# Optimization experiments

Hardware: AMD Instinct MI355X
Metric: run time of the kernel (lower is better)

## Reference

```python
import jax, jax.numpy as jnp
import numpy as np

N = 200000
D = 64
NNZ = 6400000
NUM_LAYERS = 4
CURVE = 1.0
MIN_NORM = 1e-15
EPS = 1e-7  # float32 clamp eps for arcosh domain


def logmap0_hyperboloid(x, c):
    # Lorentz-model log map at the origin (HGCN Hyperboloid.logmap0).
    # x: [N, D] points on hyperboloid; first coord is the time component.
    K = 1.0 / c
    sqrtK = K ** 0.5
    y = x[:, 1:]                                             # [N, D-1]
    y_norm = jnp.maximum(
        jnp.linalg.norm(y, axis=-1, keepdims=True), MIN_NORM)
    theta = jnp.maximum(x[:, 0:1] / sqrtK, 1.0 + EPS)
    res = sqrtK * jnp.arccosh(theta) * y / y_norm            # [N, D-1]
    return jnp.concatenate([jnp.zeros_like(x[:, :1]), res], axis=-1)


def spmm(rows, cols, vals, x):
    # COO sparse [N,N] @ dense [N,D]
    return jax.ops.segment_sum(vals[:, None] * x[cols], rows, num_segments=N)


def setup_inputs() -> dict:
    key = jax.random.key(0)
    k1, k2, k3, k4 = jax.random.split(key, 4)
    # Build valid hyperboloid points: x0 = sqrt(K + ||y||^2)
    y = jax.random.normal(k1, (N, D - 1), dtype=jnp.float32)
    K = 1.0 / CURVE
    x0 = jnp.sqrt(K + jnp.sum(y * y, axis=-1, keepdims=True))
    x = jnp.concatenate([x0, y], axis=-1)                    # [N, D]
    rows = jax.random.randint(k2, (NNZ,), 0, N, dtype=jnp.int32)
    cols = jax.random.randint(k3, (NNZ,), 0, N, dtype=jnp.int32)
    vals = jax.random.uniform(k4, (NNZ,), dtype=jnp.float32) / 32.0
    return {"x": x, "rows": rows, "cols": cols, "vals": vals}


def reference(x, rows, cols, vals):
    h = logmap0_hyperboloid(x, CURVE)
    # denseGCN: output[0]=h; output[i+1] = sum(output[1:i+1]) + A @ output[i]
    # Maintain running sum S = sum(output[1:i+1]) instead of re-summing (O(L) not O(L^2)).
    prev = h          # output[i]
    S = jnp.zeros_like(h)
    for i in range(NUM_LAYERS):
        cur = S + spmm(rows, cols, vals, prev) if i > 0 else spmm(rows, cols, vals, prev)
        S = S + cur
        prev = cur
    return prev
```

## Files before the change

### kernel.cpp

```cpp
#include <hip/hip_runtime.h>
#include <hip/hip_fp16.h>

#define SCAN_T 256
#define DELTA 512
#define LOG_DELTA 9
#define CAP 20480
#define PA_CHUNK 8192
#define MAXB 512

__global__ void compute_h_kernel(const float* __restrict__ x, __half2* __restrict__ h, int N) {
    int hw = (blockIdx.x * blockDim.x + threadIdx.x) >> 5;
    if (hw >= N) return;
    int l = threadIdx.x & 31;
    const float2* x2 = (const float2*)x;
    float2 v = x2[hw * 32 + l];
    float y2 = (l == 0) ? v.y * v.y : v.x * v.x + v.y * v.y;
    #pragma unroll
    for (int m = 16; m >= 1; m >>= 1) y2 += __shfl_xor(y2, m, 32);
    float x0 = __shfl(v.x, 0, 32);
    float ynorm = fmaxf(sqrtf(y2), 1e-15f);
    float theta = fmaxf(x0, 1.0f + 1e-7f);
    float alpha = acoshf(theta) / ynorm;
    float2 r = (l == 0) ? make_float2(0.0f, v.y * alpha)
                        : make_float2(v.x * alpha, v.y * alpha);
    h[hw * 32 + l] = __float22half2_rn(r);
}

__device__ __forceinline__ int block_incl_scan(int x) {
    __shared__ int sh[SCAN_T];
    int t = threadIdx.x;
    sh[t] = x; __syncthreads();
    for (int ofs = 1; ofs < SCAN_T; ofs <<= 1) {
        int y = (t >= ofs) ? sh[t - ofs] : 0;
        __syncthreads();
        x += y; sh[t] = x;
        __syncthreads();
    }
    return x;
}

__global__ void pass_a_kernel(const int* __restrict__ rows, const int* __restrict__ cols,
                              const float* __restrict__ vals, int* __restrict__ fill,
                              unsigned long long* __restrict__ slab, int nnz, int NB) {
    __shared__ int cnt[MAXB];
    __shared__ int cur[MAXB];
    int t = threadIdx.x;
    int start = blockIdx.x * PA_CHUNK;
    int end = min(start + PA_CHUNK, nnz);
    for (int i = t; i < NB; i += 256) cnt[i] = 0;
    __syncthreads();
    for (int e = start + t; e < end; e += 256)
        atomicAdd(&cnt[rows[e] >> LOG_DELTA], 1);
    __syncthreads();
    for (int i = t; i < NB; i += 256) {
        int c = cnt[i];
        cur[i] = (c > 0) ? atomicAdd(&fill[i], c) : 0;
    }
    __syncthreads();
    for (int e = start + t; e < end; e += 256) {
        int r = rows[e];
        int bkt = r >> LOG_DELTA;
        int lr = r & (DELTA - 1);
        int pos = atomicAdd(&cur[bkt], 1);
        if (pos < CAP) {
            unsigned long long hi = ((unsigned long long)(((unsigned)lr << 18) | (unsigned)cols[e])) << 32;
            slab[(size_t)bkt * CAP + pos] = hi | (unsigned long long)__float_as_uint(vals[e]);
        }
    }
}

__global__ void bucket_scan_kernel(const int* __restrict__ fill, int* __restrict__ csr_base,
                                   int* __restrict__ row_ptr, int NB, int N, int nnz) {
    int t = threadIdx.x;
    int a0 = (2 * t < NB) ? fill[2 * t] : 0;
    int a1 = (2 * t + 1 < NB) ? fill[2 * t + 1] : 0;
    int s = a0 + a1;
    int incl = block_incl_scan(s);
    int excl = incl - s;
    if (2 * t < NB) csr_base[2 * t] = excl;
    if (2 * t + 1 < NB) csr_base[2 * t + 1] = excl + a0;
    if (t == 0) row_ptr[N] = nnz;
}

__global__ void pass_b_kernel(const int* __restrict__ fill, const unsigned long long* __restrict__ slab,
                              const int* __restrict__ csr_base, unsigned long long* __restrict__ edges,
                              int* __restrict__ row_ptr, int N) {
    __shared__ int cnt[DELTA];
    int b = blockIdx.x;
    int t = threadIdx.x;
    cnt[t] = 0; cnt[t + 256] = 0;
    __syncthreads();
    int m = fill[b];
    if (m > CAP) m = CAP;
    const unsigned long long* sl = slab + (size_t)b * CAP;
    for (int e = t; e < m; e += 256)
        atomicAdd(&cnt[(int)(sl[e] >> 50)], 1);
    __syncthreads();
    int a0 = cnt[2 * t], a1 = cnt[2 * t + 1];
    int s = a0 + a1;
    int incl = block_incl_scan(s);
    int excl = incl - s;
    cnt[2 * t] = excl; cnt[2 * t + 1] = excl + a0;
    __syncthreads();
    int base_row = b * DELTA;
    int cb = csr_base[b];
    for (int lr = t; lr < DELTA; lr += 256) {
        int row = base_row + lr;
        if (row < N) row_ptr[row] = cb + cnt[lr];
    }
    __syncthreads();
    for (int e = t; e < m; e += 256) {
        unsigned long long u = sl[e];
        int lr = (int)(u >> 50);
        unsigned col = (unsigned)(u >> 32) & 0x3FFFFu;
        unsigned vb = (unsigned)u;
        int pos = cb + atomicAdd(&cnt[lr], 1);
        edges[pos] = ((unsigned long long)vb << 32) | col;
    }
}

__global__ void spmm_layer_kernel(const int* __restrict__ row_ptr,
                                  const unsigned long long* __restrict__ edges,
                                  const __half2* __restrict__ pin, __half2* __restrict__ pout,
                                  float2* __restrict__ out, float coef, int init_out,
                                  int store_p, int N) {
    int hw = (blockIdx.x * blockDim.x + threadIdx.x) >> 5;
    if (hw >= N) return;
    int l = threadIdx.x & 31;
    int j = row_ptr[hw];
    int end = row_ptr[hw + 1];
    float accx = 0.0f, accy = 0.0f;
    for (; j + 8 <= end; j += 8) {
        unsigned long long e0 = __builtin_nontemporal_load(&edges[j]);
        unsigned long long e1 = __builtin_nontemporal_load(&edges[j + 1]);
        unsigned long long e2 = __builtin_nontemporal_load(&edges[j + 2]);
        unsigned long long e3 = __builtin_nontemporal_load(&edges[j + 3]);
        unsigned long long e4 = __builtin_nontemporal_load(&edges[j + 4]);
        unsigned long long e5 = __builtin_nontemporal_load(&edges[j + 5]);
        unsigned long long e6 = __builtin_nontemporal_load(&edges[j + 6]);
        unsigned long long e7 = __builtin_nontemporal_load(&edges[j + 7]);
        float2 f0 = __half22float2(pin[(int)(e0 & 0xFFFFFFFFu) * 32 + l]);
        float2 f1 = __half22float2(pin[(int)(e1 & 0xFFFFFFFFu) * 32 + l]);
        float2 f2 = __half22float2(pin[(int)(e2 & 0xFFFFFFFFu) * 32 + l]);
        float2 f3 = __half22float2(pin[(int)(e3 & 0xFFFFFFFFu) * 32 + l]);
        float2 f4 = __half22float2(pin[(int)(e4 & 0xFFFFFFFFu) * 32 + l]);
        float2 f5 = __half22float2(pin[(int)(e5 & 0xFFFFFFFFu) * 32 + l]);
        float2 f6 = __half22float2(pin[(int)(e6 & 0xFFFFFFFFu) * 32 + l]);
        float2 f7 = __half22float2(pin[(int)(e7 & 0xFFFFFFFFu) * 32 + l]);
        float v0 = __int_as_float((int)(e0 >> 32)), v1 = __int_as_float((int)(e1 >> 32));
        float v2 = __int_as_float((int)(e2 >> 32)), v3 = __int_as_float((int)(e3 >> 32));
        float v4 = __int_as_float((int)(e4 >> 32)), v5 = __int_as_float((int)(e5 >> 32));
        float v6 = __int_as_float((int)(e6 >> 32)), v7 = __int_as_float((int)(e7 >> 32));
        accx = fmaf(v0, f0.x, accx); accy = fmaf(v0, f0.y, accy);
        accx = fmaf(v1, f1.x, accx); accy = fmaf(v1, f1.y, accy);
        accx = fmaf(v2, f2.x, accx); accy = fmaf(v2, f2.y, accy);
        accx = fmaf(v3, f3.x, accx); accy = fmaf(v3, f3.y, accy);
        accx = fmaf(v4, f4.x, accx); accy = fmaf(v4, f4.y, accy);
        accx = fmaf(v5, f5.x, accx); accy = fmaf(v5, f5.y, accy);
        accx = fmaf(v6, f6.x, accx); accy = fmaf(v6, f6.y, accy);
        accx = fmaf(v7, f7.x, accx); accy = fmaf(v7, f7.y, accy);
    }
    for (; j < end; ++j) {
        unsigned long long e = __builtin_nontemporal_load(&edges[j]);
        float2 f = __half22float2(pin[(int)(e & 0xFFFFFFFFu) * 32 + l]);
        float v = __int_as_float((int)(e >> 32));
        accx = fmaf(v, f.x, accx); accy = fmaf(v, f.y, accy);
    }
    int idx = hw * 32 + l;
    if (store_p) pout[idx] = __float22half2_rn(make_float2(accx, accy));
    if (init_out) {
        out[idx] = make_float2(coef * accx, coef * accy);
    } else {
        float2 o = out[idx];
        o.x = fmaf(coef, accx, o.x);
        o.y = fmaf(coef, accy, o.y);
        out[idx] = o;
    }
}

extern "C" void kernel_launch(void* const* d_in, const int* in_sizes, int n_in,
                              void* d_out, int out_size, void* d_ws, size_t ws_size,
                              hipStream_t stream) {
    const float* x    = (const float*)d_in[0];
    const int*   rows = (const int*)d_in[1];
    const int*   cols = (const int*)d_in[2];
    const float* vals = (const float*)d_in[3];
    float2* out = (float2*)d_out;
    const int D = 64;
    const int N = in_sizes[0] / D;
    const int nnz = in_sizes[1];
    const int NB = (N + DELTA - 1) / DELTA;

    char* ws = (char*)d_ws;
    size_t off = 0;
    auto alloc = [&](size_t bytes) -> void* {
        void* p = ws + off;
        off = (off + bytes + 255) & ~(size_t)255;
        return p;
    };
    int*     fill     = (int*)alloc((size_t)MAXB * 4);
    int*     csr_base = (int*)alloc((size_t)MAXB * 4);
    int*     row_ptr  = (int*)alloc((size_t)(N + 1) * 4);
    unsigned long long* slab  = (unsigned long long*)alloc((size_t)NB * CAP * 8);
    unsigned long long* edges = (unsigned long long*)alloc((size_t)nnz * 8);
    __half2* pA = (__half2*)alloc((size_t)N * D * 2);
    __half2* pB = (__half2*)alloc((size_t)N * D * 2);
    (void)ws_size; (void)n_in; (void)out_size;

    hipMemsetAsync(fill, 0, (size_t)MAXB * 4, stream);

    const int rblocks = (N + 7) / 8;
    compute_h_kernel<<<rblocks, 256, 0, stream>>>(x, pA, N);

    int pa_blocks = (nnz + PA_CHUNK - 1) / PA_CHUNK;
    pass_a_kernel<<<pa_blocks, 256, 0, stream>>>(rows, cols, vals, fill, slab, nnz, NB);
    bucket_scan_kernel<<<1, 256, 0, stream>>>(fill, csr_base, row_ptr, NB, N, nnz);
    pass_b_kernel<<<NB, 256, 0, stream>>>(fill, slab, csr_base, edges, row_ptr, N);

    spmm_layer_kernel<<<rblocks, 256, 0, stream>>>(row_ptr, edges, pA, pB, out, 4.0f, 1, 1, N);
    spmm_layer_kernel<<<rblocks, 256, 0, stream>>>(row_ptr, edges, pB, pA, out, 5.0f, 0, 1, N);
    spmm_layer_kernel<<<rblocks, 256, 0, stream>>>(row_ptr, edges, pA, pB, out, 3.0f, 0, 1, N);
    spmm_layer_kernel<<<rblocks, 256, 0, stream>>>(row_ptr, edges, pB, pA, out, 1.0f, 0, 0, N);
}
```

Measured before the change: 1.027 ms.

## Sort edges by column phase within rows and fuse output accumulation into final layer

Pass B now bins each row's edges by a coarse column range (32 phases), so edges within a row are ordered by column region. Neighbouring rows processed at the same time then gather from similar parts of the feature table, which should improve cache locality. The per-layer fp32 output read-modify-write is removed: the intermediate half-precision layer results are kept in three buffers, and the final kernel combines them with coefficients 4, 5 and 3. The cost is a 16K-entry shared-memory histogram with a serial 64-element scan per thread, plus one extra workspace buffer.

```diff
diff --git a/kernel.cpp b/kernel.cpp
--- a/kernel.cpp
+++ b/kernel.cpp
@@ -7,6 +7,10 @@
 #define CAP 20480
 #define PA_CHUNK 8192
 #define MAXB 512
+#define NPH 32
+#define PHSHIFT 13
+
+typedef unsigned long long u64;
 
 __global__ void compute_h_kernel(const float* __restrict__ x, __half2* __restrict__ h, int N) {
     int hw = (blockIdx.x * blockDim.x + threadIdx.x) >> 5;
@@ -41,7 +45,7 @@
 
 __global__ void pass_a_kernel(const int* __restrict__ rows, const int* __restrict__ cols,
                               const float* __restrict__ vals, int* __restrict__ fill,
-                              unsigned long long* __restrict__ slab, int nnz, int NB) {
+                              u64* __restrict__ slab, int nnz, int NB) {
     __shared__ int cnt[MAXB];
     __shared__ int cur[MAXB];
     int t = threadIdx.x;
@@ -63,8 +67,8 @@
         int lr = r & (DELTA - 1);
         int pos = atomicAdd(&cur[bkt], 1);
         if (pos < CAP) {
-            unsigned long long hi = ((unsigned long long)(((unsigned)lr << 18) | (unsigned)cols[e])) << 32;
-            slab[(size_t)bkt * CAP + pos] = hi | (unsigned long long)__float_as_uint(vals[e]);
+            u64 hi = ((u64)(((unsigned)lr << 18) | (unsigned)cols[e])) << 32;
+            slab[(size_t)bkt * CAP + pos] = hi | (u64)__float_as_uint(vals[e]);
         }
     }
 }
@@ -82,63 +86,65 @@
     if (t == 0) row_ptr[N] = nnz;
 }
 
-__global__ void pass_b_kernel(const int* __restrict__ fill, const unsigned long long* __restrict__ slab,
-                              const int* __restrict__ csr_base, unsigned long long* __restrict__ edges,
+__global__ void pass_b_kernel(const int* __restrict__ fill, const u64* __restrict__ slab,
+                              const int* __restrict__ csr_base, u64* __restrict__ edges,
                               int* __restrict__ row_ptr, int N) {
-    __shared__ int cnt[DELTA];
+    __shared__ int bins[DELTA * NPH];
     int b = blockIdx.x;
     int t = threadIdx.x;
-    cnt[t] = 0; cnt[t + 256] = 0;
+    for (int i = t; i < DELTA * NPH; i += 256) bins[i] = 0;
     __syncthreads();
     int m = fill[b];
     if (m > CAP) m = CAP;
-    const unsigned long long* sl = slab + (size_t)b * CAP;
-    for (int e = t; e < m; e += 256)
-        atomicAdd(&cnt[(int)(sl[e] >> 50)], 1);
-    __syncthreads();
-    int a0 = cnt[2 * t], a1 = cnt[2 * t + 1];
-    int s = a0 + a1;
+    const u64* sl = slab + (size_t)b * CAP;
+    for (int e = t; e < m; e += 256) {
+        u64 u = sl[e];
+        int lr = (int)(u >> 50);
+        int col = (int)((u >> 32) & 0x3FFFFu);
+        atomicAdd(&bins[lr * NPH + (col >> PHSHIFT)], 1);
+    }
+    __syncthreads();
+    int base = t * 64;
+    int s = 0;
+    #pragma unroll 4
+    for (int k = 0; k < 64; ++k) s += bins[base + k];
     int incl = block_incl_scan(s);
-    int excl = incl - s;
-    cnt[2 * t] = excl; cnt[2 * t + 1] = excl + a0;
-    __syncthreads();
+    int run = incl - s;
+    for (int k = 0; k < 64; ++k) { int c = bins[base + k]; bins[base + k] = run; run += c; }
+    __syncthreads();
+    int cb = csr_base[b];
     int base_row = b * DELTA;
-    int cb = csr_base[b];
     for (int lr = t; lr < DELTA; lr += 256) {
         int row = base_row + lr;
-        if (row < N) row_ptr[row] = cb + cnt[lr];
+        if (row < N) row_ptr[row] = cb + bins[lr * NPH];
     }
     __syncthreads();
     for (int e = t; e < m; e += 256) {
-        unsigned long long u = sl[e];
+        u64 u = sl[e];
         int lr = (int)(u >> 50);
         unsigned col = (unsigned)(u >> 32) & 0x3FFFFu;
         unsigned vb = (unsigned)u;
-        int pos = cb + atomicAdd(&cnt[lr], 1);
-        edges[pos] = ((unsigned long long)vb << 32) | col;
-    }
-}
-
-__global__ void spmm_layer_kernel(const int* __restrict__ row_ptr,
-                                  const unsigned long long* __restrict__ edges,
-                                  const __half2* __restrict__ pin, __half2* __restrict__ pout,
-                                  float2* __restrict__ out, float coef, int init_out,
-                                  int store_p, int N) {
-    int hw = (blockIdx.x * blockDim.x + threadIdx.x) >> 5;
-    if (hw >= N) return;
-    int l = threadIdx.x & 31;
+        int pos = cb + atomicAdd(&bins[lr * NPH + (int)(col >> PHSHIFT)], 1);
+        edges[pos] = ((u64)vb << 32) | col;
+    }
+}
+
+__device__ __forceinline__ void spmm_row(const int* __restrict__ row_ptr,
+                                         const u64* __restrict__ edges,
+                                         const __half2* __restrict__ pin,
+                                         int hw, int l, float& accx, float& accy) {
     int j = row_ptr[hw];
     int end = row_ptr[hw + 1];
-    float accx = 0.0f, accy = 0.0f;
+    accx = 0.0f; accy = 0.0f;
     for (; j + 8 <= end; j += 8) {
-        unsigned long long e0 = __builtin_nontemporal_load(&edges[j]);
-        unsigned long long e1 = __builtin_nontemporal_load(&edges[j + 1]);
-        unsigned long long e2 = __builtin_nontemporal_load(&edges[j + 2]);
-        unsigned long long e3 = __builtin_nontemporal_load(&edges[j + 3]);
-        unsigned long long e4 = __builtin_nontemporal_load(&edges[j + 4]);
-        unsigned long long e5 = __builtin_nontemporal_load(&edges[j + 5]);
-        unsigned long long e6 = __builtin_nontemporal_load(&edges[j + 6]);
-        unsigned long long e7 = __builtin_nontemporal_load(&edges[j + 7]);
+        u64 e0 = __builtin_nontemporal_load(&edges[j]);
+        u64 e1 = __builtin_nontemporal_load(&edges[j + 1]);
+        u64 e2 = __builtin_nontemporal_load(&edges[j + 2]);
+        u64 e3 = __builtin_nontemporal_load(&edges[j + 3]);
+        u64 e4 = __builtin_nontemporal_load(&edges[j + 4]);
+        u64 e5 = __builtin_nontemporal_load(&edges[j + 5]);
+        u64 e6 = __builtin_nontemporal_load(&edges[j + 6]);
+        u64 e7 = __builtin_nontemporal_load(&edges[j + 7]);
         float2 f0 = __half22float2(pin[(int)(e0 & 0xFFFFFFFFu) * 32 + l]);
         float2 f1 = __half22float2(pin[(int)(e1 & 0xFFFFFFFFu) * 32 + l]);
         float2 f2 = __half22float2(pin[(int)(e2 & 0xFFFFFFFFu) * 32 + l]);
@@ -161,21 +167,38 @@
         accx = fmaf(v7, f7.x, accx); accy = fmaf(v7, f7.y, accy);
     }
     for (; j < end; ++j) {
-        unsigned long long e = __builtin_nontemporal_load(&edges[j]);
+        u64 e = __builtin_nontemporal_load(&edges[j]);
         float2 f = __half22float2(pin[(int)(e & 0xFFFFFFFFu) * 32 + l]);
         float v = __int_as_float((int)(e >> 32));
         accx = fmaf(v, f.x, accx); accy = fmaf(v, f.y, accy);
     }
+}
+
+__global__ void spmm_kernel(const int* __restrict__ row_ptr, const u64* __restrict__ edges,
+                            const __half2* __restrict__ pin, __half2* __restrict__ pout, int N) {
+    int hw = (blockIdx.x * blockDim.x + threadIdx.x) >> 5;
+    if (hw >= N) return;
+    int l = threadIdx.x & 31;
+    float accx, accy;
+    spmm_row(row_ptr, edges, pin, hw, l, accx, accy);
+    pout[hw * 32 + l] = __float22half2_rn(make_float2(accx, accy));
+}
+
+__global__ void spmm_final_kernel(const int* __restrict__ row_ptr, const u64* __restrict__ edges,
+                                  const __half2* __restrict__ p1, const __half2* __restrict__ p2,
+                                  const __half2* __restrict__ p3, float2* __restrict__ out, int N) {
+    int hw = (blockIdx.x * blockDim.x + threadIdx.x) >> 5;
+    if (hw >= N) return;
+    int l = threadIdx.x & 31;
+    float accx, accy;
+    spmm_row(row_ptr, edges, p3, hw, l, accx, accy);
     int idx = hw * 32 + l;
-    if (store_p) pout[idx] = __float22half2_rn(make_float2(accx, accy));
-    if (init_out) {
-        out[idx] = make_float2(coef * accx, coef * accy);
-    } else {
-        float2 o = out[idx];
-        o.x = fmaf(coef, accx, o.x);
-        o.y = fmaf(coef, accy, o.y);
-        out[idx] = o;
-    }
+    float2 f1 = __half22float2(p1[idx]);
+    float2 f2 = __half22float2(p2[idx]);
+    float2 f3 = __half22float2(p3[idx]);
+    float ox = fmaf(4.0f, f1.x, fmaf(5.0f, f2.x, fmaf(3.0f, f3.x, accx)));
+    float oy = fmaf(4.0f, f1.y, fmaf(5.0f, f2.y, fmaf(3.0f, f3.y, accy)));
+    out[idx] = make_float2(ox, oy);
 }
 
 extern "C" void kernel_launch(void* const* d_in, const int* in_sizes, int n_in,
@@ -201,24 +224,25 @@
     int*     fill     = (int*)alloc((size_t)MAXB * 4);
     int*     csr_base = (int*)alloc((size_t)MAXB * 4);
     int*     row_ptr  = (int*)alloc((size_t)(N + 1) * 4);
-    unsigned long long* slab  = (unsigned long long*)alloc((size_t)NB * CAP * 8);
-    unsigned long long* edges = (unsigned long long*)alloc((size_t)nnz * 8);
-    __half2* pA = (__half2*)alloc((size_t)N * D * 2);
-    __half2* pB = (__half2*)alloc((size_t)N * D * 2);
+    u64*     slab     = (u64*)alloc((size_t)NB * CAP * 8);
+    u64*     edges    = (u64*)alloc((size_t)nnz * 8);
+    __half2* B0 = (__half2*)alloc((size_t)N * D * 2);
+    __half2* B1 = (__half2*)alloc((size_t)N * D * 2);
+    __half2* B2 = (__half2*)alloc((size_t)N * D * 2);
     (void)ws_size; (void)n_in; (void)out_size;
 
     hipMemsetAsync(fill, 0, (size_t)MAXB * 4, stream);
 
     const int rblocks = (N + 7) / 8;
-    compute_h_kernel<<<rblocks, 256, 0, stream>>>(x, pA, N);
+    compute_h_kernel<<<rblocks, 256, 0, stream>>>(x, B0, N);
 
     int pa_blocks = (nnz + PA_CHUNK - 1) / PA_CHUNK;
     pass_a_kernel<<<pa_blocks, 256, 0, stream>>>(rows, cols, vals, fill, slab, nnz, NB);
     bucket_scan_kernel<<<1, 256, 0, stream>>>(fill, csr_base, row_ptr, NB, N, nnz);
     pass_b_kernel<<<NB, 256, 0, stream>>>(fill, slab, csr_base, edges, row_ptr, N);
 
-    spmm_layer_kernel<<<rblocks, 256, 0, stream>>>(row_ptr, edges, pA, pB, out, 4.0f, 1, 1, N);
-    spmm_layer_kernel<<<rblocks, 256, 0, stream>>>(row_ptr, edges, pB, pA, out, 5.0f, 0, 1, N);
-    spmm_layer_kernel<<<rblocks, 256, 0, stream>>>(row_ptr, edges, pA, pB, out, 3.0f, 0, 1, N);
-    spmm_layer_kernel<<<rblocks, 256, 0, stream>>>(row_ptr, edges, pB, pA, out, 1.0f, 0, 0, N);
-}
+    spmm_kernel<<<rblocks, 256, 0, stream>>>(row_ptr, edges, B0, B1, N);
+    spmm_kernel<<<rblocks, 256, 0, stream>>>(row_ptr, edges, B1, B2, N);
+    spmm_kernel<<<rblocks, 256, 0, stream>>>(row_ptr, edges, B2, B0, N);
+    spmm_final_kernel<<<rblocks, 256, 0, stream>>>(row_ptr, edges, B1, B2, B0, out, N);
+}
```

New measurement: 1.022 ms. About the same (-0.5%).
